# Kernel optimization log

Measured on AMD Instinct MI355X. Metric: run time of the kernel, lower is better.

## Reference

```python
import jax, jax.numpy as jnp
import numpy as np

N, M, D, K = 32768, 8192, 384, 9


def setup_inputs() -> dict:
    key = jax.random.key(0)
    k1, k2 = jax.random.split(key)
    return {
        "embedding": jax.random.normal(k1, (N, D), dtype=jnp.float32),
        "memory_bank": jax.random.normal(k2, (M, D), dtype=jnp.float32),
        "n_neighbors": K,
    }


def reference(embedding, memory_bank, n_neighbors):
    x_norm = jnp.sum(embedding * embedding, axis=-1, keepdims=True)      # [N, 1]
    y_norm = jnp.sum(memory_bank * memory_bank, axis=-1, keepdims=True)  # [M, 1]
    d2 = x_norm - 2.0 * jnp.matmul(embedding, memory_bank.T) + y_norm.T  # [N, M]
    dist = jnp.sqrt(jnp.maximum(d2, 0.0))
    # topk smallest along dim 1 (patch_scores, indices discarded)
    neg_top, _ = jax.lax.top_k(-dist, n_neighbors)
    patch_scores = -neg_top  # [N, K], ascending distances
    return patch_scores
```

## Files before the change

kernel.cpp:

```cpp
#include <hip/hip_runtime.h>
#include <hip/hip_bf16.h>

#define N_ROWS 32768
#define M_ROWS 8192
#define D_DIM  384
#define K_NB   9
#define BN     64
#define BM     256
#define MQ     (M_ROWS / 4)
#define TILES  (MQ / BN)
#define KS     3

#define QSCALE (1.0f / 2048.0f)
#define YOFF   0.125f
#define QSTEPF (2048.0f / 65535.0f)
#define QOFFB  256.0f
#define M2S    (-2.0f / 2048.0f)
#define BIGF   3.0e38f

#define YS_OFF 49152

typedef __attribute__((ext_vector_type(4))) int      i32x4;
typedef __attribute__((ext_vector_type(8))) int      i32x8;
typedef __attribute__((ext_vector_type(4))) float    f32x4;
typedef __attribute__((ext_vector_type(4))) unsigned u32x4;

#define GLDS(SRC, DST)                                                       \
  __builtin_amdgcn_global_load_lds(                                          \
      (const __attribute__((address_space(1))) void*)(SRC),                  \
      (__attribute__((address_space(3))) void*)(DST), 16, 0, 0)

__global__ __launch_bounds__(256) void FAPM_prep8(
    const float* __restrict__ emb, const float* __restrict__ mem,
    unsigned* __restrict__ A8, unsigned* __restrict__ B8,
    float* __restrict__ xn, float* __restrict__ yn) {
  const int lane = threadIdx.x & 63;
  const int row  = blockIdx.x * 4 + (threadIdx.x >> 6);
  const float* src;
  unsigned* dst;
  float* nptr;
  if (row < N_ROWS) {
    src = emb + (size_t)row * D_DIM; dst = A8 + (size_t)row * 96; nptr = xn + row;
  } else {
    int r = row - N_ROWS;
    src = mem + (size_t)r * D_DIM; dst = B8 + (size_t)r * 96; nptr = yn + r;
  }
  float s = 0.f;
  {
    int dw = lane;
    f32x4 v = *(const f32x4*)(src + dw * 4);
    s += v.x * v.x + v.y * v.y + v.z * v.z + v.w * v.w;
    int pk = __builtin_amdgcn_cvt_pk_fp8_f32(v.x, v.y, 0, false);
    pk = __builtin_amdgcn_cvt_pk_fp8_f32(v.z, v.w, pk, true);
    dst[dw] = (unsigned)pk;
  }
  if (lane < 32) {
    int dw = lane + 64;
    f32x4 v = *(const f32x4*)(src + dw * 4);
    s += v.x * v.x + v.y * v.y + v.z * v.z + v.w * v.w;
    int pk = __builtin_amdgcn_cvt_pk_fp8_f32(v.x, v.y, 0, false);
    pk = __builtin_amdgcn_cvt_pk_fp8_f32(v.z, v.w, pk, true);
    dst[dw] = (unsigned)pk;
  }
#pragma unroll
  for (int dd = 1; dd < 64; dd <<= 1) s += __shfl_xor(s, dd);
  if (lane == 0) *nptr = s;
}

__device__ __forceinline__ unsigned pkmin(unsigned a, unsigned b) {
  unsigned d;
  asm("v_pk_min_u16 %0, %1, %2" : "=v"(d) : "v"(a), "v"(b));
  return d;
}
__device__ __forceinline__ unsigned pkmax(unsigned a, unsigned b) {
  unsigned d;
  asm("v_pk_max_u16 %0, %1, %2" : "=v"(d) : "v"(a), "v"(b));
  return d;
}

__device__ __forceinline__ void merge16i(unsigned t[9], float* dst, int sub) {
  for (int s = 0; s < K_NB; ++s) {
    unsigned m  = t[0];
    int      ml = sub;
#pragma unroll
    for (int dd = 1; dd < 16; dd <<= 1) {
      unsigned ov = (unsigned)__shfl_xor((int)m, dd);
      int      ol = __shfl_xor(ml, dd);
      bool take = (ov < m) || (ov == m && ol < ml);
      m  = take ? ov : m;
      ml = take ? ol : ml;
    }
    if (sub == ml) {
#pragma unroll
      for (int j = 0; j < 8; ++j) t[j] = t[j + 1];
      t[8] = 0xFFFFu;
    }
    if (sub == 0) dst[s] = (float)m * QSTEPF - QOFFB;
  }
}

__global__ __launch_bounds__(256, 2) void FAPM_fused(
    const unsigned char* __restrict__ A8, const unsigned char* __restrict__ B8,
    const float* __restrict__ yn, float* __restrict__ part) {
  __shared__ __attribute__((aligned(128))) unsigned char LDS[53248];
  const int tid  = threadIdx.x;
  const int lane = tid & 63;
  const int w    = tid >> 6;
  const int sub  = lane & 15;
  const int grp  = lane >> 4;
  const int bx   = blockIdx.x;
  const int mq   = bx & 3;
  const int row0 = (bx >> 2) * BM;
  const int colbase = mq * MQ;

  {
    const float* yp = yn + colbase + tid * 8;
    f32x4 v0 = *(const f32x4*)yp;
    f32x4 v1 = *(const f32x4*)(yp + 4);
    float a0 = fmaf(v0.x, QSCALE, YOFF), a1 = fmaf(v0.y, QSCALE, YOFF);
    float a2 = fmaf(v0.z, QSCALE, YOFF), a3 = fmaf(v0.w, QSCALE, YOFF);
    float a4 = fmaf(v1.x, QSCALE, YOFF), a5 = fmaf(v1.y, QSCALE, YOFF);
    float a6 = fmaf(v1.z, QSCALE, YOFF), a7 = fmaf(v1.w, QSCALE, YOFF);
    unsigned q0, q1, q2, q3;
    asm("v_cvt_pknorm_u16_f32 %0, %1, %2" : "=v"(q0) : "v"(a0), "v"(a1));
    asm("v_cvt_pknorm_u16_f32 %0, %1, %2" : "=v"(q1) : "v"(a2), "v"(a3));
    asm("v_cvt_pknorm_u16_f32 %0, %1, %2" : "=v"(q2) : "v"(a4), "v"(a5));
    asm("v_cvt_pknorm_u16_f32 %0, %1, %2" : "=v"(q3) : "v"(a6), "v"(a7));
    *(u32x4*)(&LDS[YS_OFF + tid * 16]) = (u32x4){q0, q1, q2, q3};
  }

  i32x8 af[4][KS];

#pragma unroll
  for (int half = 0; half < 2; ++half) {
    const unsigned char* asrc =
        A8 + (size_t)(row0 + half * 128 + (w * 2) * 16 + (lane & 15)) * D_DIM +
        (lane >> 4) * 32;
#pragma unroll
    for (int rb2 = 0; rb2 < 2; ++rb2)
#pragma unroll
      for (int ks = 0; ks < KS; ++ks)
#pragma unroll
        for (int h = 0; h < 2; ++h)
          GLDS(asrc + rb2 * 16 * D_DIM + ks * 128 + h * 16,
               LDS + (((w * 2 + rb2) * KS + ks) * 2 + h) * 1024);
    asm volatile("s_waitcnt vmcnt(0)" ::: "memory");
    __syncthreads();
    if ((w >> 1) == half) {
      const int rbh = (w & 1) * 4;
#pragma unroll
      for (int rbl = 0; rbl < 4; ++rbl)
#pragma unroll
        for (int ks = 0; ks < KS; ++ks) {
          const unsigned char* p =
              LDS + (((rbh + rbl) * KS + ks) * 2) * 1024 + lane * 16;
          *(i32x4*)&af[rbl][ks] = *(const i32x4*)p;
          *((i32x4*)&af[rbl][ks] + 1) = *(const i32x4*)(p + 1024);
        }
    }
    __syncthreads();
  }

  const unsigned char* bsrc =
      B8 + (size_t)(colbase + w * 16 + (lane & 15)) * D_DIM + (lane >> 4) * 32;
#pragma unroll
  for (int ks = 0; ks < KS; ++ks)
#pragma unroll
    for (int h = 0; h < 2; ++h)
      GLDS(bsrc + ks * 128 + h * 16, LDS + w * 6144 + (ks * 2 + h) * 1024);
#pragma unroll
  for (int ks = 0; ks < KS; ++ks)
#pragma unroll
    for (int h = 0; h < 2; ++h)
      GLDS(bsrc + 24576 + ks * 128 + h * 16,
           LDS + 24576 + w * 6144 + (ks * 2 + h) * 1024);
  bsrc += 2 * 24576;

  unsigned tkp[2][4][9];
#pragma unroll
  for (int s2 = 0; s2 < 2; ++s2)
#pragma unroll
    for (int i = 0; i < 4; ++i)
#pragma unroll
      for (int j = 0; j < 9; ++j) tkp[s2][i][j] = 0xFFFFFFFFu;

  for (int t = 0; t < TILES; ++t) {
    const int bufo = (t & 1) * 24576;
    if (t + 1 < TILES) asm volatile("s_waitcnt vmcnt(6)" ::: "memory");
    else               asm volatile("s_waitcnt vmcnt(0)" ::: "memory");
    __builtin_amdgcn_s_barrier();

    const unsigned char* br = LDS + bufo + lane * 16;
#pragma unroll
    for (int cb = 0; cb < 4; ++cb) {
      unsigned yu = *(const unsigned short*)(
          &LDS[YS_OFF + ((t * 64 + cb * 16 + sub) << 1)]);
      float ysv = (float)yu * (1.0f / 65535.0f);

      i32x8 bf[KS];
#pragma unroll
      for (int ks = 0; ks < KS; ++ks) {
        const unsigned char* p = br + cb * 6144 + ks * 2048;
        *(i32x4*)&bf[ks] = *(const i32x4*)p;
        *((i32x4*)&bf[ks] + 1) = *(const i32x4*)(p + 1024);
      }
      f32x4 acc[4];
#pragma unroll
      for (int rbl = 0; rbl < 4; ++rbl) acc[rbl] = (f32x4){0.f, 0.f, 0.f, 0.f};
      __builtin_amdgcn_s_setprio(1);
#pragma unroll
      for (int ks = 0; ks < KS; ++ks)
#pragma unroll
        for (int rbl = 0; rbl < 4; ++rbl)
          acc[rbl] = __builtin_amdgcn_mfma_scale_f32_16x16x128_f8f6f4(
              af[rbl][ks], bf[ks], acc[rbl], 0, 0,
              0, 0x7F7F7F7F, 0, 0x7F7F7F7F);
      __builtin_amdgcn_s_setprio(0);

#pragma unroll
      for (int s2 = 0; s2 < 2; ++s2)
#pragma unroll
        for (int i = 0; i < 4; ++i) {
          float d2a = fmaf(acc[2 * s2][i], M2S, ysv);
          float d2b = fmaf(acc[2 * s2 + 1][i], M2S, ysv);
          unsigned dp;
          asm("v_cvt_pknorm_u16_f32 %0, %1, %2" : "=v"(dp) : "v"(d2a), "v"(d2b));
#pragma unroll
          for (int j = 8; j >= 1; --j)
            tkp[s2][i][j] = pkmin(tkp[s2][i][j], pkmax(dp, tkp[s2][i][j - 1]));
          tkp[s2][i][0] = pkmin(tkp[s2][i][0], dp);
        }
    }
    __builtin_amdgcn_s_barrier();

    if (t + 2 < TILES) {
#pragma unroll
      for (int ks = 0; ks < KS; ++ks)
#pragma unroll
        for (int h = 0; h < 2; ++h)
          GLDS(bsrc + ks * 128 + h * 16,
               LDS + bufo + w * 6144 + (ks * 2 + h) * 1024);
      bsrc += 24576;
    }
  }

  float* pbase = part + (size_t)mq * N_ROWS * K_NB;
#pragma unroll
  for (int s2 = 0; s2 < 2; ++s2)
#pragma unroll
    for (int i = 0; i < 4; ++i) {
      unsigned ta[9], tb[9];
#pragma unroll
      for (int j = 0; j < 9; ++j) {
        ta[j] = tkp[s2][i][j] & 0xFFFFu;
        tb[j] = tkp[s2][i][j] >> 16;
      }
      int rowA = row0 + w * 64 + (2 * s2) * 16 + grp * 4 + i;
      merge16i(ta, pbase + (size_t)rowA * K_NB, sub);
      merge16i(tb, pbase + (size_t)(rowA + 16) * K_NB, sub);
    }
}

__global__ __launch_bounds__(256) void FAPM_merge4(
    const float* __restrict__ part, const float* __restrict__ xn,
    float* __restrict__ out) {
  const int r = blockIdx.x * 256 + threadIdx.x;
  const float xr = xn[r];
  float l[4][9];
#pragma unroll
  for (int q = 0; q < 4; ++q)
#pragma unroll
    for (int j = 0; j < 9; ++j)
      l[q][j] = part[(size_t)q * N_ROWS * K_NB + (size_t)r * K_NB + j];
#pragma unroll
  for (int s = 0; s < K_NB; ++s) {
    float m = fminf(fminf(l[0][0], l[1][0]), fminf(l[2][0], l[3][0]));
    out[(size_t)r * K_NB + s] = sqrtf(fmaxf(m + xr, 0.f));
    bool t0 = (l[0][0] == m);
    bool t1 = (l[1][0] == m) && !t0;
    bool t2 = (l[2][0] == m) && !t0 && !t1;
    bool t3 = !(t0 || t1 || t2);
#pragma unroll
    for (int j = 0; j < 8; ++j) {
      l[0][j] = t0 ? l[0][j + 1] : l[0][j];
      l[1][j] = t1 ? l[1][j + 1] : l[1][j];
      l[2][j] = t2 ? l[2][j + 1] : l[2][j];
      l[3][j] = t3 ? l[3][j + 1] : l[3][j];
    }
    l[0][8] = t0 ? BIGF : l[0][8];
    l[1][8] = t1 ? BIGF : l[1][8];
    l[2][8] = t2 ? BIGF : l[2][8];
    l[3][8] = t3 ? BIGF : l[3][8];
  }
}

extern "C" void kernel_launch(void* const* d_in, const int* in_sizes, int n_in,
                              void* d_out, int out_size, void* d_ws, size_t ws_size,
                              hipStream_t stream) {
  const float* emb = (const float*)d_in[0];
  const float* mem = (const float*)d_in[1];
  float* out = (float*)d_out;
  char* ws = (char*)d_ws;
  size_t offA = 0;
  size_t offB = offA + (size_t)N_ROWS * D_DIM;
  size_t offX = offB + (size_t)M_ROWS * D_DIM;
  size_t offY = offX + (size_t)N_ROWS * 4;
  size_t offP = offY + (size_t)M_ROWS * 4;
  unsigned char* A8 = (unsigned char*)(ws + offA);
  unsigned char* B8 = (unsigned char*)(ws + offB);
  float* xn = (float*)(ws + offX);
  float* yn = (float*)(ws + offY);
  float* part = (float*)(ws + offP);

  FAPM_prep8<<<(N_ROWS + M_ROWS) / 4, 256, 0, stream>>>(
      emb, mem, (unsigned*)A8, (unsigned*)B8, xn, yn);
  FAPM_fused<<<(N_ROWS / BM) * 4, 256, 0, stream>>>(A8, B8, yn, part);
  FAPM_merge4<<<N_ROWS / 256, 256, 0, stream>>>(part, xn, out);
}
```

Before: 192.5 us.

## Use triple-buffered B ring and software-pipeline MFMA with top-k updates

Replaces the double-buffered B tile with a three-slot LDS ring. The next prefetch is now issued right after the barrier, and the second per-tile barrier is removed. The per-tile inner loop is restructured so MFMAs for the next column block are issued before the top-k insertion for the previous block, interleaving matrix work with VALU min/max chains. LDS use rises to about 76 KB per block, which may limit occupancy against the 2-blocks-per-CU launch bound. More accumulators are live at once, raising register pressure.

```diff
diff --git a/kernel.cpp b/kernel.cpp
--- a/kernel.cpp
+++ b/kernel.cpp
@@ -7,7 +7,8 @@
 #define K_NB   9
 #define BN     64
 #define BM     256
-#define MQ     (M_ROWS / 4)
+#define NMQ    4
+#define MQ     (M_ROWS / NMQ)
 #define TILES  (MQ / BN)
 #define KS     3
 
@@ -18,7 +19,9 @@
 #define M2S    (-2.0f / 2048.0f)
 #define BIGF   3.0e38f
 
-#define YS_OFF 49152
+#define BUFSZ  24576
+#define RING   3
+#define YS_OFF 73728
 
 typedef __attribute__((ext_vector_type(4))) int      i32x4;
 typedef __attribute__((ext_vector_type(8))) int      i32x8;
@@ -29,6 +32,10 @@
   __builtin_amdgcn_global_load_lds(                                          \
       (const __attribute__((address_space(1))) void*)(SRC),                  \
       (__attribute__((address_space(3))) void*)(DST), 16, 0, 0)
+
+#define MF(AF, B, C)                                                         \
+  __builtin_amdgcn_mfma_scale_f32_16x16x128_f8f6f4(                          \
+      (AF), (B), (C), 0, 0, 0, 0x7F7F7F7F, 0, 0x7F7F7F7F)
 
 __global__ __launch_bounds__(256) void FAPM_prep8(
     const float* __restrict__ emb, const float* __restrict__ mem,
@@ -99,17 +106,64 @@
   }
 }
 
+__device__ __forceinline__ void topk_update(
+    const f32x4& a0, const f32x4& a1, const f32x4& a2, const f32x4& a3,
+    float ysv, unsigned tkp[2][4][9]) {
+#pragma unroll
+  for (int i = 0; i < 4; ++i) {
+    {
+      float d2a = fmaf(a0[i], M2S, ysv);
+      float d2b = fmaf(a1[i], M2S, ysv);
+      unsigned dp;
+      asm("v_cvt_pknorm_u16_f32 %0, %1, %2" : "=v"(dp) : "v"(d2a), "v"(d2b));
+#pragma unroll
+      for (int j = 8; j >= 1; --j)
+        tkp[0][i][j] = pkmin(tkp[0][i][j], pkmax(dp, tkp[0][i][j - 1]));
+      tkp[0][i][0] = pkmin(tkp[0][i][0], dp);
+    }
+    {
+      float d2a = fmaf(a2[i], M2S, ysv);
+      float d2b = fmaf(a3[i], M2S, ysv);
+      unsigned dp;
+      asm("v_cvt_pknorm_u16_f32 %0, %1, %2" : "=v"(dp) : "v"(d2a), "v"(d2b));
+#pragma unroll
+      for (int j = 8; j >= 1; --j)
+        tkp[1][i][j] = pkmin(tkp[1][i][j], pkmax(dp, tkp[1][i][j - 1]));
+      tkp[1][i][0] = pkmin(tkp[1][i][0], dp);
+    }
+  }
+}
+
+#define MFMA_SET(A0, A1, A2, A3, CB)                                         \
+  {                                                                          \
+    i32x8 _b;                                                                \
+    __builtin_amdgcn_s_setprio(1);                                           \
+    *(i32x4*)&_b = *(const i32x4*)(br + (CB) * 6144);                        \
+    *((i32x4*)&_b + 1) = *(const i32x4*)(br + (CB) * 6144 + 1024);           \
+    A0 = MF(af[0][0], _b, Z); A1 = MF(af[1][0], _b, Z);                      \
+    A2 = MF(af[2][0], _b, Z); A3 = MF(af[3][0], _b, Z);                      \
+    *(i32x4*)&_b = *(const i32x4*)(br + (CB) * 6144 + 2048);                 \
+    *((i32x4*)&_b + 1) = *(const i32x4*)(br + (CB) * 6144 + 3072);           \
+    A0 = MF(af[0][1], _b, A0); A1 = MF(af[1][1], _b, A1);                    \
+    A2 = MF(af[2][1], _b, A2); A3 = MF(af[3][1], _b, A3);                    \
+    *(i32x4*)&_b = *(const i32x4*)(br + (CB) * 6144 + 4096);                 \
+    *((i32x4*)&_b + 1) = *(const i32x4*)(br + (CB) * 6144 + 5120);           \
+    A0 = MF(af[0][2], _b, A0); A1 = MF(af[1][2], _b, A1);                    \
+    A2 = MF(af[2][2], _b, A2); A3 = MF(af[3][2], _b, A3);                    \
+    __builtin_amdgcn_s_setprio(0);                                           \
+  }
+
 __global__ __launch_bounds__(256, 2) void FAPM_fused(
     const unsigned char* __restrict__ A8, const unsigned char* __restrict__ B8,
     const float* __restrict__ yn, float* __restrict__ part) {
-  __shared__ __attribute__((aligned(128))) unsigned char LDS[53248];
+  __shared__ __attribute__((aligned(128))) unsigned char LDS[77824];
   const int tid  = threadIdx.x;
   const int lane = tid & 63;
   const int w    = tid >> 6;
   const int sub  = lane & 15;
   const int grp  = lane >> 4;
   const int bx   = blockIdx.x;
-  const int mq   = bx & 3;
+  const int mq   = bx & (NMQ - 1);
   const int row0 = (bx >> 2) * BM;
   const int colbase = mq * MQ;
 
@@ -134,8 +188,7 @@
 #pragma unroll
   for (int half = 0; half < 2; ++half) {
     const unsigned char* asrc =
-        A8 + (size_t)(row0 + half * 128 + (w * 2) * 16 + (lane & 15)) * D_DIM +
-        (lane >> 4) * 32;
+        A8 + (size_t)(row0 + half * 128 + (w * 2) * 16 + sub) * D_DIM + grp * 32;
 #pragma unroll
     for (int rb2 = 0; rb2 < 2; ++rb2)
 #pragma unroll
@@ -162,7 +215,7 @@
   }
 
   const unsigned char* bsrc =
-      B8 + (size_t)(colbase + w * 16 + (lane & 15)) * D_DIM + (lane >> 4) * 32;
+      B8 + (size_t)(colbase + w * 16 + sub) * D_DIM + grp * 32;
 #pragma unroll
   for (int ks = 0; ks < KS; ++ks)
 #pragma unroll
@@ -172,9 +225,9 @@
   for (int ks = 0; ks < KS; ++ks)
 #pragma unroll
     for (int h = 0; h < 2; ++h)
-      GLDS(bsrc + 24576 + ks * 128 + h * 16,
-           LDS + 24576 + w * 6144 + (ks * 2 + h) * 1024);
-  bsrc += 2 * 24576;
+      GLDS(bsrc + BUFSZ + ks * 128 + h * 16,
+           LDS + BUFSZ + w * 6144 + (ks * 2 + h) * 1024);
+  bsrc += 2 * BUFSZ;
 
   unsigned tkp[2][4][9];
 #pragma unroll
@@ -184,64 +237,45 @@
 #pragma unroll
       for (int j = 0; j < 9; ++j) tkp[s2][i][j] = 0xFFFFFFFFu;
 
+  const f32x4 Z = {0.f, 0.f, 0.f, 0.f};
+  int bufR = 0;
+  int bufW = 2 * BUFSZ;
+
   for (int t = 0; t < TILES; ++t) {
-    const int bufo = (t & 1) * 24576;
     if (t + 1 < TILES) asm volatile("s_waitcnt vmcnt(6)" ::: "memory");
     else               asm volatile("s_waitcnt vmcnt(0)" ::: "memory");
     __builtin_amdgcn_s_barrier();
-
-    const unsigned char* br = LDS + bufo + lane * 16;
+    if (t + 2 < TILES) {
+#pragma unroll
+      for (int ks = 0; ks < KS; ++ks)
+#pragma unroll
+        for (int h = 0; h < 2; ++h)
+          GLDS(bsrc + ks * 128 + h * 16,
+               LDS + bufW + w * 6144 + (ks * 2 + h) * 1024);
+      bsrc += BUFSZ;
+    }
+
+    float ysv[4];
 #pragma unroll
     for (int cb = 0; cb < 4; ++cb) {
       unsigned yu = *(const unsigned short*)(
           &LDS[YS_OFF + ((t * 64 + cb * 16 + sub) << 1)]);
-      float ysv = (float)yu * (1.0f / 65535.0f);
-
-      i32x8 bf[KS];
-#pragma unroll
-      for (int ks = 0; ks < KS; ++ks) {
-        const unsigned char* p = br + cb * 6144 + ks * 2048;
-        *(i32x4*)&bf[ks] = *(const i32x4*)p;
-        *((i32x4*)&bf[ks] + 1) = *(const i32x4*)(p + 1024);
-      }
-      f32x4 acc[4];
-#pragma unroll
-      for (int rbl = 0; rbl < 4; ++rbl) acc[rbl] = (f32x4){0.f, 0.f, 0.f, 0.f};
-      __builtin_amdgcn_s_setprio(1);
-#pragma unroll
-      for (int ks = 0; ks < KS; ++ks)
-#pragma unroll
-        for (int rbl = 0; rbl < 4; ++rbl)
-          acc[rbl] = __builtin_amdgcn_mfma_scale_f32_16x16x128_f8f6f4(
-              af[rbl][ks], bf[ks], acc[rbl], 0, 0,
-              0, 0x7F7F7F7F, 0, 0x7F7F7F7F);
-      __builtin_amdgcn_s_setprio(0);
-
-#pragma unroll
-      for (int s2 = 0; s2 < 2; ++s2)
-#pragma unroll
-        for (int i = 0; i < 4; ++i) {
-          float d2a = fmaf(acc[2 * s2][i], M2S, ysv);
-          float d2b = fmaf(acc[2 * s2 + 1][i], M2S, ysv);
-          unsigned dp;
-          asm("v_cvt_pknorm_u16_f32 %0, %1, %2" : "=v"(dp) : "v"(d2a), "v"(d2b));
-#pragma unroll
-          for (int j = 8; j >= 1; --j)
-            tkp[s2][i][j] = pkmin(tkp[s2][i][j], pkmax(dp, tkp[s2][i][j - 1]));
-          tkp[s2][i][0] = pkmin(tkp[s2][i][0], dp);
-        }
-    }
-    __builtin_amdgcn_s_barrier();
-
-    if (t + 2 < TILES) {
-#pragma unroll
-      for (int ks = 0; ks < KS; ++ks)
-#pragma unroll
-        for (int h = 0; h < 2; ++h)
-          GLDS(bsrc + ks * 128 + h * 16,
-               LDS + bufo + w * 6144 + (ks * 2 + h) * 1024);
-      bsrc += 24576;
-    }
+      ysv[cb] = (float)yu * (1.0f / 65535.0f);
+    }
+
+    const unsigned char* br = LDS + bufR + lane * 16;
+    f32x4 A0, A1, A2, A3, B0, B1, B2, B3;
+    MFMA_SET(A0, A1, A2, A3, 0);
+    MFMA_SET(B0, B1, B2, B3, 1);
+    topk_update(A0, A1, A2, A3, ysv[0], tkp);
+    MFMA_SET(A0, A1, A2, A3, 2);
+    topk_update(B0, B1, B2, B3, ysv[1], tkp);
+    MFMA_SET(B0, B1, B2, B3, 3);
+    topk_update(A0, A1, A2, A3, ysv[2], tkp);
+    topk_update(B0, B1, B2, B3, ysv[3], tkp);
+
+    bufR += BUFSZ; if (bufR == RING * BUFSZ) bufR = 0;
+    bufW += BUFSZ; if (bufW == RING * BUFSZ) bufW = 0;
   }
 
   float* pbase = part + (size_t)mq * N_ROWS * K_NB;
@@ -314,6 +348,6 @@
 
   FAPM_prep8<<<(N_ROWS + M_ROWS) / 4, 256, 0, stream>>>(
       emb, mem, (unsigned*)A8, (unsigned*)B8, xn, yn);
-  FAPM_fused<<<(N_ROWS / BM) * 4, 256, 0, stream>>>(A8, B8, yn, part);
+  FAPM_fused<<<(N_ROWS / BM) * NMQ, 256, 0, stream>>>(A8, B8, yn, part);
   FAPM_merge4<<<N_ROWS / 256, 256, 0, stream>>>(part, xn, out);
 }
```

Result: no change. 195.9 us (+1.8%).

## Load B operands directly from global into registers, dropping LDS double-buffer

Applied to the files above, without the earlier changes.

Removes the LDS double-buffered staging of memory-bank tiles and the per-tile barriers. Each wave now loads its B fragments straight from global memory (L2-resident) into registers, software-pipelined one k-slice ahead of the MFMAs. This trades cross-wave LDS sharing and synchronisation for redundant global/L2 traffic (all four waves now fetch the same B data) and exposed load latency.

```diff
diff --git a/kernel.cpp b/kernel.cpp
--- a/kernel.cpp
+++ b/kernel.cpp
@@ -5,10 +5,9 @@
 #define M_ROWS 8192
 #define D_DIM  384
 #define K_NB   9
-#define BN     64
 #define BM     256
 #define MQ     (M_ROWS / 4)
-#define TILES  (MQ / BN)
+#define NCB    (MQ / 16)
 #define KS     3
 
 #define QSCALE (1.0f / 2048.0f)
@@ -29,6 +28,10 @@
   __builtin_amdgcn_global_load_lds(                                          \
       (const __attribute__((address_space(1))) void*)(SRC),                  \
       (__attribute__((address_space(3))) void*)(DST), 16, 0, 0)
+
+#define MF(AF, B, C)                                                         \
+  __builtin_amdgcn_mfma_scale_f32_16x16x128_f8f6f4(                          \
+      (AF), (B), (C), 0, 0, 0, 0x7F7F7F7F, 0, 0x7F7F7F7F)
 
 __global__ __launch_bounds__(256) void FAPM_prep8(
     const float* __restrict__ emb, const float* __restrict__ mem,
@@ -99,6 +102,43 @@
   }
 }
 
+#define LOADB(DST, P, OFS)                                                   \
+  {                                                                          \
+    *(i32x4*)&(DST)       = *(const i32x4*)((P) + (OFS));                    \
+    *((i32x4*)&(DST) + 1) = *(const i32x4*)((P) + (OFS) + 16);               \
+  }
+
+#define MFMA4(B, KSI)                                                        \
+  {                                                                          \
+    __builtin_amdgcn_s_setprio(1);                                           \
+    acc0 = MF(af[0][KSI], (B), acc0);                                        \
+    acc1 = MF(af[1][KSI], (B), acc1);                                        \
+    acc2 = MF(af[2][KSI], (B), acc2);                                        \
+    acc3 = MF(af[3][KSI], (B), acc3);                                        \
+    __builtin_amdgcn_s_setprio(0);                                           \
+  }
+
+#define TOPK()                                                               \
+  {                                                                          \
+    unsigned yu = *(const unsigned short*)(                                  \
+        &LDS[YS_OFF + ((c * 16 + sub) << 1)]);                               \
+    float ysv = (float)yu * (1.0f / 65535.0f);                               \
+    const f32x4* ac[4] = {&acc0, &acc1, &acc2, &acc3};                       \
+    _Pragma("unroll")                                                        \
+    for (int s2 = 0; s2 < 2; ++s2)                                           \
+      _Pragma("unroll")                                                      \
+      for (int i = 0; i < 4; ++i) {                                          \
+        float d2a = fmaf((*ac[2 * s2])[i], M2S, ysv);                        \
+        float d2b = fmaf((*ac[2 * s2 + 1])[i], M2S, ysv);                    \
+        unsigned dp;                                                         \
+        asm("v_cvt_pknorm_u16_f32 %0, %1, %2" : "=v"(dp) : "v"(d2a), "v"(d2b)); \
+        _Pragma("unroll")                                                    \
+        for (int j = 8; j >= 1; --j)                                         \
+          tkp[s2][i][j] = pkmin(tkp[s2][i][j], pkmax(dp, tkp[s2][i][j - 1]));\
+        tkp[s2][i][0] = pkmin(tkp[s2][i][0], dp);                            \
+      }                                                                      \
+  }
+
 __global__ __launch_bounds__(256, 2) void FAPM_fused(
     const unsigned char* __restrict__ A8, const unsigned char* __restrict__ B8,
     const float* __restrict__ yn, float* __restrict__ part) {
@@ -134,8 +174,7 @@
 #pragma unroll
   for (int half = 0; half < 2; ++half) {
     const unsigned char* asrc =
-        A8 + (size_t)(row0 + half * 128 + (w * 2) * 16 + (lane & 15)) * D_DIM +
-        (lane >> 4) * 32;
+        A8 + (size_t)(row0 + half * 128 + (w * 2) * 16 + sub) * D_DIM + grp * 32;
 #pragma unroll
     for (int rb2 = 0; rb2 < 2; ++rb2)
 #pragma unroll
@@ -161,21 +200,6 @@
     __syncthreads();
   }
 
-  const unsigned char* bsrc =
-      B8 + (size_t)(colbase + w * 16 + (lane & 15)) * D_DIM + (lane >> 4) * 32;
-#pragma unroll
-  for (int ks = 0; ks < KS; ++ks)
-#pragma unroll
-    for (int h = 0; h < 2; ++h)
-      GLDS(bsrc + ks * 128 + h * 16, LDS + w * 6144 + (ks * 2 + h) * 1024);
-#pragma unroll
-  for (int ks = 0; ks < KS; ++ks)
-#pragma unroll
-    for (int h = 0; h < 2; ++h)
-      GLDS(bsrc + 24576 + ks * 128 + h * 16,
-           LDS + 24576 + w * 6144 + (ks * 2 + h) * 1024);
-  bsrc += 2 * 24576;
-
   unsigned tkp[2][4][9];
 #pragma unroll
   for (int s2 = 0; s2 < 2; ++s2)
@@ -184,64 +208,33 @@
 #pragma unroll
       for (int j = 0; j < 9; ++j) tkp[s2][i][j] = 0xFFFFFFFFu;
 
-  for (int t = 0; t < TILES; ++t) {
-    const int bufo = (t & 1) * 24576;
-    if (t + 1 < TILES) asm volatile("s_waitcnt vmcnt(6)" ::: "memory");
-    else               asm volatile("s_waitcnt vmcnt(0)" ::: "memory");
-    __builtin_amdgcn_s_barrier();
-
-    const unsigned char* br = LDS + bufo + lane * 16;
-#pragma unroll
-    for (int cb = 0; cb < 4; ++cb) {
-      unsigned yu = *(const unsigned short*)(
-          &LDS[YS_OFF + ((t * 64 + cb * 16 + sub) << 1)]);
-      float ysv = (float)yu * (1.0f / 65535.0f);
-
-      i32x8 bf[KS];
-#pragma unroll
-      for (int ks = 0; ks < KS; ++ks) {
-        const unsigned char* p = br + cb * 6144 + ks * 2048;
-        *(i32x4*)&bf[ks] = *(const i32x4*)p;
-        *((i32x4*)&bf[ks] + 1) = *(const i32x4*)(p + 1024);
-      }
-      f32x4 acc[4];
-#pragma unroll
-      for (int rbl = 0; rbl < 4; ++rbl) acc[rbl] = (f32x4){0.f, 0.f, 0.f, 0.f};
-      __builtin_amdgcn_s_setprio(1);
-#pragma unroll
-      for (int ks = 0; ks < KS; ++ks)
-#pragma unroll
-        for (int rbl = 0; rbl < 4; ++rbl)
-          acc[rbl] = __builtin_amdgcn_mfma_scale_f32_16x16x128_f8f6f4(
-              af[rbl][ks], bf[ks], acc[rbl], 0, 0,
-              0, 0x7F7F7F7F, 0, 0x7F7F7F7F);
-      __builtin_amdgcn_s_setprio(0);
-
-#pragma unroll
-      for (int s2 = 0; s2 < 2; ++s2)
-#pragma unroll
-        for (int i = 0; i < 4; ++i) {
-          float d2a = fmaf(acc[2 * s2][i], M2S, ysv);
-          float d2b = fmaf(acc[2 * s2 + 1][i], M2S, ysv);
-          unsigned dp;
-          asm("v_cvt_pknorm_u16_f32 %0, %1, %2" : "=v"(dp) : "v"(d2a), "v"(d2b));
-#pragma unroll
-          for (int j = 8; j >= 1; --j)
-            tkp[s2][i][j] = pkmin(tkp[s2][i][j], pkmax(dp, tkp[s2][i][j - 1]));
-          tkp[s2][i][0] = pkmin(tkp[s2][i][0], dp);
-        }
-    }
-    __builtin_amdgcn_s_barrier();
-
-    if (t + 2 < TILES) {
-#pragma unroll
-      for (int ks = 0; ks < KS; ++ks)
-#pragma unroll
-        for (int h = 0; h < 2; ++h)
-          GLDS(bsrc + ks * 128 + h * 16,
-               LDS + bufo + w * 6144 + (ks * 2 + h) * 1024);
-      bsrc += 24576;
-    }
+  const unsigned char* bq = B8 + (size_t)(colbase + sub) * D_DIM + grp * 32;
+  i32x8 b0, b1, b2;
+  LOADB(b0, bq, 0);
+  LOADB(b1, bq, 128);
+
+  for (int c = 0; c < NCB - 1; ++c) {
+    const unsigned char* bp = bq + (size_t)c * 6144;
+    f32x4 acc0 = {0.f,0.f,0.f,0.f}, acc1 = {0.f,0.f,0.f,0.f};
+    f32x4 acc2 = {0.f,0.f,0.f,0.f}, acc3 = {0.f,0.f,0.f,0.f};
+    LOADB(b2, bp, 256);
+    MFMA4(b0, 0);
+    LOADB(b0, bp, 6144);
+    MFMA4(b1, 1);
+    LOADB(b1, bp, 6272);
+    MFMA4(b2, 2);
+    TOPK();
+  }
+  {
+    const int c = NCB - 1;
+    const unsigned char* bp = bq + (size_t)c * 6144;
+    f32x4 acc0 = {0.f,0.f,0.f,0.f}, acc1 = {0.f,0.f,0.f,0.f};
+    f32x4 acc2 = {0.f,0.f,0.f,0.f}, acc3 = {0.f,0.f,0.f,0.f};
+    LOADB(b2, bp, 256);
+    MFMA4(b0, 0);
+    MFMA4(b1, 1);
+    MFMA4(b2, 2);
+    TOPK();
   }
 
   float* pbase = part + (size_t)mq * N_ROWS * K_NB;
```

Result: slower. 232.5 us (+20.8%).
